# Optimization experiments

Hardware: AMD Instinct MI355X
Metric: run time of the kernel (lower is better)

The kernel has to match this reference:

```python
import jax, jax.numpy as jnp
import numpy as np

B, S, H, NH = 2, 1024, 1024, 16
SE, E = 512, 1024
NEXP, TOPK, FF = 8, 2, 2048
HD = H // NH
EPS = 1e-6
THETA = 10000.0
NEG = -1e9


def _rms(x, w):
    return x * jax.lax.rsqrt(jnp.mean(x * x, axis=-1, keepdims=True) + EPS) * w


def _rope(q, k, pos):
    # q,k: [B,S,NH,HD]; pos: [B,S] int
    inv = 1.0 / (THETA ** (jnp.arange(0, HD, 2, dtype=jnp.float32) / HD))
    f = pos[..., None].astype(jnp.float32) * inv            # [B,S,HD/2]
    emb = jnp.concatenate([f, f], axis=-1)                  # [B,S,HD]
    cos = jnp.cos(emb)[:, :, None, :]
    sin = jnp.sin(emb)[:, :, None, :]
    def rot(x):
        x1, x2 = jnp.split(x, 2, axis=-1)
        return jnp.concatenate([-x2, x1], axis=-1)
    return q * cos + rot(q) * sin, k * cos + rot(k) * sin


def _forward(hidden_states, encoder_hidden_states,
             in_ln_w, wq, wk, wv, wo,
             c_norm_w, cq_w, cq_b, ck_w, ck_b, cv_w, cv_b, co_w, co_b,
             post_ln_w, gate_w, w1, w2, w3,
             position_ids, encoder_attention_mask):
    x = hidden_states

    # ---- self-attention (RMSNorm pre-norm, RoPE, causal) ----
    res = x
    h = _rms(x, in_ln_w)
    q = (h @ wq.T).reshape(B, S, NH, HD)
    k = (h @ wk.T).reshape(B, S, NH, HD)
    v = (h @ wv.T).reshape(B, S, NH, HD)
    q, k = _rope(q, k, position_ids)
    scores = jnp.einsum('bqhd,bkhd->bhqk', q, k) / np.sqrt(HD)
    causal = jnp.tril(jnp.ones((S, S), dtype=bool))
    scores = jnp.where(causal, scores, NEG)
    attn = jax.nn.softmax(scores, axis=-1)
    o = jnp.einsum('bhqk,bkhd->bqhd', attn, v).reshape(B, S, H) @ wo.T
    x = res + o

    # ---- cross-attention block (RMSNorm, MHA with kdim=vdim=E, bias) ----
    res = x
    h = _rms(x, c_norm_w)
    cq = (h @ cq_w.T + cq_b).reshape(B, S, NH, HD)
    ck = (encoder_hidden_states @ ck_w.T + ck_b).reshape(B, SE, NH, HD)
    cv = (encoder_hidden_states @ cv_w.T + cv_b).reshape(B, SE, NH, HD)
    sc = jnp.einsum('bqhd,bkhd->bhqk', cq, ck) / np.sqrt(HD)
    pad = (encoder_attention_mask == 0)                     # key_padding_mask
    sc = jnp.where(pad[:, None, None, :], NEG, sc)
    ca = jax.nn.softmax(sc, axis=-1)
    o = jnp.einsum('bhqk,bkhd->bqhd', ca, cv).reshape(B, S, H) @ co_w.T + co_b
    x = res + o

    # ---- block-sparse MoE FFN (top-2 routing, SwiGLU experts) ----
    res = x
    h = _rms(x, post_ln_w).reshape(-1, H)                   # [T,H], T=B*S
    logits = h @ gate_w.T                                    # [T,NEXP]
    probs = jax.nn.softmax(logits, axis=-1)
    topv, topi = jax.lax.top_k(probs, TOPK)                  # [T,TOPK]
    topv = topv / jnp.sum(topv, axis=-1, keepdims=True)
    out = jnp.zeros_like(h)
    for e in range(NEXP):  # fixed small expert loop
        we = jnp.sum(jnp.where(topi == e, topv, 0.0), axis=-1)   # [T]
        ff = (jax.nn.silu(h @ w1[e].T) * (h @ w3[e].T)) @ w2[e].T
        out = out + we[:, None] * ff
    x = res + out.reshape(B, S, H)
    return x


def setup_inputs() -> dict:
    key = jax.random.key(0)
    ks = jax.random.split(key, 24)
    sc = 0.02
    d = {
        'hidden_states': jax.random.normal(ks[0], (B, S, H), jnp.float32),
        'position_ids': jnp.broadcast_to(jnp.arange(S, dtype=jnp.int64), (B, S)),
        'encoder_hidden_states': jax.random.normal(ks[1], (B, SE, E), jnp.float32),
        'encoder_attention_mask': jnp.ones((B, SE), jnp.int64),
        'in_ln_w': jnp.ones((H,), jnp.float32),
        'wq': jax.random.normal(ks[2], (H, H), jnp.float32) * sc,
        'wk': jax.random.normal(ks[3], (H, H), jnp.float32) * sc,
        'wv': jax.random.normal(ks[4], (H, H), jnp.float32) * sc,
        'wo': jax.random.normal(ks[5], (H, H), jnp.float32) * sc,
        'c_norm_w': jnp.ones((H,), jnp.float32),
        'cq_w': jax.random.normal(ks[6], (H, H), jnp.float32) * sc,
        'cq_b': jnp.zeros((H,), jnp.float32),
        'ck_w': jax.random.normal(ks[7], (H, E), jnp.float32) * sc,
        'ck_b': jnp.zeros((H,), jnp.float32),
        'cv_w': jax.random.normal(ks[8], (H, E), jnp.float32) * sc,
        'cv_b': jnp.zeros((H,), jnp.float32),
        'co_w': jax.random.normal(ks[9], (H, H), jnp.float32) * sc,
        'co_b': jnp.zeros((H,), jnp.float32),
        'post_ln_w': jnp.ones((H,), jnp.float32),
        'gate_w': jax.random.normal(ks[10], (NEXP, H), jnp.float32) * sc,
        'w1': jax.random.normal(ks[11], (NEXP, FF, H), jnp.float32) * sc,
        'w2': jax.random.normal(ks[12], (NEXP, H, FF), jnp.float32) * sc,
        'w3': jax.random.normal(ks[13], (NEXP, FF, H), jnp.float32) * sc,
    }
    return d


def reference(hidden_states, position_ids, encoder_hidden_states, encoder_attention_mask,
              in_ln_w, wq, wk, wv, wo,
              c_norm_w, cq_w, cq_b, ck_w, ck_b, cv_w, cv_b, co_w, co_b,
              post_ln_w, gate_w, w1, w2, w3):
    return _forward(hidden_states, encoder_hidden_states,
                    in_ln_w, wq, wk, wv, wo,
                    c_norm_w, cq_w, cq_b, ck_w, ck_b, cv_w, cv_b, co_w, co_b,
                    post_ln_w, gate_w, w1, w2, w3,
                    position_ids, encoder_attention_mask)
```

## Files before the change

### kernel.cpp

```cpp
#include <hip/hip_runtime.h>

#define B_    2
#define S_    1024
#define H_    1024
#define NH_   16
#define HD_   64
#define SE_   512
#define E_    1024
#define NEXP_ 8
#define FF_   2048
#define T_    (B_*S_)
#define TE_   (B_*SE_)
#define PERM_MAX 6400
#define MAXRT 24

typedef short v8s __attribute__((ext_vector_type(8)));
typedef short v4s __attribute__((ext_vector_type(4)));
typedef float v4f __attribute__((ext_vector_type(4)));
typedef _Float16 v8h __attribute__((ext_vector_type(8)));
typedef _Float16 v4h __attribute__((ext_vector_type(4)));

__device__ __forceinline__ unsigned short f2b(float f) {
  unsigned int u = __float_as_uint(f);
  u = (u + 0x7FFFu + ((u >> 16) & 1u)) >> 16;
  return (unsigned short)u;
}

__device__ __forceinline__ void g2l16(const void* g, void* l) {
  __builtin_amdgcn_global_load_lds(
      (const __attribute__((address_space(1))) unsigned int*)g,
      (__attribute__((address_space(3))) unsigned int*)l, 16, 0, 0);
}

__global__ void detect_kern(const int* __restrict__ pos, const int* __restrict__ msk,
                            int* __restrict__ flags, int* __restrict__ counts) {
  if (threadIdx.x < 16) counts[threadIdx.x] = 0;
  if (threadIdx.x == 0) {
    flags[0] = (pos[1] == 1) ? 0 : 1;
    flags[1] = (msk[1] == 1) ? 0 : 1;
  }
}

struct SplitArgs {
  const float* src[9];
  _Float16* dh[9];
  _Float16* dl[9];
};
__global__ __launch_bounds__(256)
void split_all(SplitArgs sa) {
  int b = blockIdx.x;
  int seg, i;
  if (b < 4096) { seg = b >> 9; i = (b & 511) * 256 + threadIdx.x; }
  else          { seg = 8;      i = (b - 4096) * 256 + threadIdx.x; }
  const float* x = sa.src[seg];
  v4f a = *(const v4f*)&x[i * 8];
  v4f c = *(const v4f*)&x[i * 8 + 4];
  v8h hv, lv;
  #pragma unroll
  for (int j = 0; j < 8; ++j) {
    float v = j < 4 ? a[j] : c[j - 4];
    _Float16 hh = (_Float16)v;
    hv[j] = hh; lv[j] = (_Float16)(v - (float)hh);
  }
  *(v8h*)&sa.dh[seg][i * 8] = hv;
  *(v8h*)&sa.dl[seg][i * 8] = lv;
}

__global__ __launch_bounds__(256)
void rmsnorm_hl_kern(const float* __restrict__ x, const float* __restrict__ w,
                     _Float16* __restrict__ yh, _Float16* __restrict__ yl) {
  int row = blockIdx.x, tid = threadIdx.x;
  const float* xr = x + (long)row * 1024;
  v4f v = *(const v4f*)&xr[tid * 4];
  float ss = v[0]*v[0] + v[1]*v[1] + v[2]*v[2] + v[3]*v[3];
  #pragma unroll
  for (int off = 32; off; off >>= 1) ss += __shfl_xor(ss, off);
  __shared__ float sw[4];
  if ((tid & 63) == 0) sw[tid >> 6] = ss;
  __syncthreads();
  float tot = sw[0] + sw[1] + sw[2] + sw[3];
  float rs = rsqrtf(tot * (1.0f / 1024.0f) + 1e-6f);
  const float* wr = w + tid * 4;
  v4h oh, ol;
  #pragma unroll
  for (int j = 0; j < 4; ++j) {
    float f = v[j] * rs * wr[j];
    _Float16 hh = (_Float16)f;
    oh[j] = hh; ol[j] = (_Float16)(f - (float)hh);
  }
  *(v4h*)&yh[(long)row * 1024 + tid * 4] = oh;
  *(v4h*)&yl[(long)row * 1024 + tid * 4] = ol;
}

__global__ __launch_bounds__(256)
void rmsnorm_kern(const float* __restrict__ x, const float* __restrict__ w,
                  unsigned short* __restrict__ y) {
  int row = blockIdx.x, tid = threadIdx.x;
  const float* xr = x + (long)row * 1024;
  v4f v = *(const v4f*)&xr[tid * 4];
  float ss = v[0]*v[0] + v[1]*v[1] + v[2]*v[2] + v[3]*v[3];
  #pragma unroll
  for (int off = 32; off; off >>= 1) ss += __shfl_xor(ss, off);
  __shared__ float sw[4];
  if ((tid & 63) == 0) sw[tid >> 6] = ss;
  __syncthreads();
  float tot = sw[0] + sw[1] + sw[2] + sw[3];
  float rs = rsqrtf(tot * (1.0f / 1024.0f) + 1e-6f);
  const float* wr = w + tid * 4;
  v4s o;
  #pragma unroll
  for (int j = 0; j < 4; ++j) o[j] = (short)f2b(v[j] * rs * wr[j]);
  *(v4s*)&y[(long)row * 1024 + tid * 4] = o;
}

__global__ __launch_bounds__(256)
void rope_split_kern(float* __restrict__ q, const float* __restrict__ k,
                     _Float16* __restrict__ kh, _Float16* __restrict__ kl,
                     const int* __restrict__ pos, const int* __restrict__ flags) {
  int g = blockIdx.x * 256 + threadIdx.x;
  int d = g & 31;
  int h = (g >> 5) & 15;
  int s = (g >> 9) & (S_ - 1);
  int b = g >> 19;
  long base = (((long)(b * S_ + s)) * NH_ + h) * HD_;
  int pidx = b * S_ + s;
  int pv = pos[flags[0] ? (pidx << 1) : pidx];
  float p = (float)pv;
  float inv = powf(10000.0f, -(float)d * (1.0f / 32.0f));
  float f = p * inv;
  float sn = sinf(f), cs = cosf(f);
  float q1 = q[base + d], q2 = q[base + d + 32];
  q[base + d]      = q1 * cs - q2 * sn;
  q[base + d + 32] = q2 * cs + q1 * sn;
  float k1 = k[base + d], k2 = k[base + d + 32];
  float kr1 = k1 * cs - k2 * sn;
  float kr2 = k2 * cs + k1 * sn;
  _Float16 hh = (_Float16)kr1;
  kh[base + d] = hh; kl[base + d] = (_Float16)(kr1 - (float)hh);
  hh = (_Float16)kr2;
  kh[base + d + 32] = hh; kl[base + d + 32] = (_Float16)(kr2 - (float)hh);
}

__global__ __launch_bounds__(256)
void vtrans_kern(const float* __restrict__ vf, _Float16* __restrict__ vth,
                 _Float16* __restrict__ vtl, int Sk) {
  int kb = blockIdx.x, bh = blockIdx.y;
  int b = bh >> 4, h = bh & 15;
  int t = threadIdx.x;
  __shared__ float tile[64][65];
  int key = t >> 2, dsub = (t & 3) * 16;
  const float* src = vf + (((long)(b * Sk + kb * 64 + key)) * NH_ + h) * HD_ + dsub;
  #pragma unroll
  for (int j = 0; j < 16; j += 4) *(v4f*)&tile[key][dsub + j] = *(const v4f*)&src[j];
  __syncthreads();
  int d = t >> 2, ksub = (t & 3) * 16;
  v8h hv0, lv0, hv1, lv1;
  #pragma unroll
  for (int j = 0; j < 16; ++j) {
    float v = tile[ksub + j][d];
    _Float16 hh = (_Float16)v;
    if (j < 8) { hv0[j] = hh; lv0[j] = (_Float16)(v - (float)hh); }
    else       { hv1[j - 8] = hh; lv1[j - 8] = (_Float16)(v - (float)hh); }
  }
  long ob = (((long)(b * NH_ + h)) * HD_ + d) * Sk + kb * 64 + ksub;
  *(v8h*)&vth[ob] = hv0; *(v8h*)&vth[ob + 8] = hv1;
  *(v8h*)&vtl[ob] = lv0; *(v8h*)&vtl[ob + 8] = lv1;
}

struct ZArg {
  const _Float16 *Ah, *Al, *Bh, *Bl;
  const float *bias, *resid;
  float *Cf;
  float *Cf2;
  _Float16 *Ch, *Cl;
  int M;
};

__global__ __launch_bounds__(256)
void gemm_hl(ZArg z0, ZArg z1, ZArg z2, int K) {
  ZArg za = blockIdx.z == 0 ? z0 : (blockIdx.z == 1 ? z1 : z2);
  int flat = blockIdx.x;
  int wg = (flat & 7) * 32 + (flat >> 3);
  int row0 = (wg >> 4) * 128;
  int col0 = (wg & 15) * 64;
  if (row0 >= za.M) return;
  int tid = threadIdx.x, lane = tid & 63, w = tid >> 6;
  int lr = lane & 15, lg = lane >> 4;
  int wr = w >> 1, wc = w & 1;
  int rsw = (lr >> 1) & 3;

  __shared__ _Float16 Ah_s[2][128 * 32], Al_s[2][128 * 32];
  __shared__ _Float16 Bh_s[2][64 * 32], Bl_s[2][64 * 32];

  int av0 = w * 64 + lane, av1 = (w + 4) * 64 + lane;
  int ar0 = av0 >> 2, as0 = (av0 & 3) ^ ((ar0 >> 1) & 3);
  int ar1 = av1 >> 2, as1 = (av1 & 3) ^ ((ar1 >> 1) & 3);
  int bv = w * 64 + lane;
  int br = bv >> 2, bs = (bv & 3) ^ ((br >> 1) & 3);
  const _Float16* ga0h = za.Ah + (long)(row0 + ar0) * K + as0 * 8;
  const _Float16* ga0l = za.Al + (long)(row0 + ar0) * K + as0 * 8;
  const _Float16* ga1h = za.Ah + (long)(row0 + ar1) * K + as1 * 8;
  const _Float16* ga1l = za.Al + (long)(row0 + ar1) * K + as1 * 8;
  const _Float16* gbh  = za.Bh + (long)(col0 + br) * K + bs * 8;
  const _Float16* gbl  = za.Bl + (long)(col0 + br) * K + bs * 8;

  auto stage = [&](int buf, int k0) {
    g2l16(ga0h + k0, (char*)Ah_s[buf] + w * 1024);
    g2l16(ga1h + k0, (char*)Ah_s[buf] + (w + 4) * 1024);
    g2l16(ga0l + k0, (char*)Al_s[buf] + w * 1024);
    g2l16(ga1l + k0, (char*)Al_s[buf] + (w + 4) * 1024);
    g2l16(gbh + k0, (char*)Bh_s[buf] + w * 1024);
    g2l16(gbl + k0, (char*)Bl_s[buf] + w * 1024);
  };

  v4f acc[4][2] = {};
  stage(0, 0);
  int cur = 0;

  for (int k0 = 0; k0 < K; k0 += 32) {
    __syncthreads();
    if (k0 + 32 < K) stage(cur ^ 1, k0 + 32);

    v8h ah[4], al[4], bh[2], bl[2];
    #pragma unroll
    for (int m = 0; m < 4; ++m) {
      int off = (wr * 64 + m * 16 + lr) * 64 + ((lg ^ rsw) << 4);
      ah[m] = *(const v8h*)((char*)Ah_s[cur] + off);
      al[m] = *(const v8h*)((char*)Al_s[cur] + off);
    }
    #pragma unroll
    for (int n = 0; n < 2; ++n) {
      int off = (wc * 32 + n * 16 + lr) * 64 + ((lg ^ rsw) << 4);
      bh[n] = *(const v8h*)((char*)Bh_s[cur] + off);
      bl[n] = *(const v8h*)((char*)Bl_s[cur] + off);
    }
    #pragma unroll
    for (int m = 0; m < 4; ++m)
      #pragma unroll
      for (int n = 0; n < 2; ++n) {
        acc[m][n] = __builtin_amdgcn_mfma_f32_16x16x32_f16(ah[m], bh[n], acc[m][n], 0, 0, 0);
        acc[m][n] = __builtin_amdgcn_mfma_f32_16x16x32_f16(ah[m], bl[n], acc[m][n], 0, 0, 0);
        acc[m][n] = __builtin_amdgcn_mfma_f32_16x16x32_f16(al[m], bh[n], acc[m][n], 0, 0, 0);
      }
    cur ^= 1;
  }

  #pragma unroll
  for (int m = 0; m < 4; ++m) {
    int rbase = row0 + wr * 64 + m * 16 + lg * 4;
    #pragma unroll
    for (int n = 0; n < 2; ++n) {
      int gcol = col0 + wc * 32 + n * 16 + lr;
      float bb = za.bias ? za.bias[gcol] : 0.0f;
      #pragma unroll
      for (int rr = 0; rr < 4; ++rr) {
        long idx = (long)(rbase + rr) * 1024 + gcol;
        float v = acc[m][n][rr] + bb;
        if (za.Cf) {
          float r = za.resid ? (za.resid[idx] + v) : v;
          za.Cf[idx] = r;
          if (za.Cf2) za.Cf2[idx] = r;
        } else {
          _Float16 hh = (_Float16)v;
          za.Ch[idx] = hh;
          za.Cl[idx] = (_Float16)(v - (float)hh);
        }
      }
    }
  }
}

template<bool CAUSAL>
__global__ __launch_bounds__(256)
void attn_hl(const float* __restrict__ Q,
             const _Float16* __restrict__ Khg, const _Float16* __restrict__ Klg,
             const _Float16* __restrict__ Vhg, const _Float16* __restrict__ Vlg,
             _Float16* __restrict__ Oh, _Float16* __restrict__ Ol,
             const int* __restrict__ mask, const int* __restrict__ flags,
             int Sq, int Sk, float qscale) {
  int flat = blockIdx.x;
  int wgA = (flat & 7) * 64 + (flat >> 3);
  int qt = wgA & 15, bh = wgA >> 4;
  int b = bh >> 4, h = bh & 15;
  int tid = threadIdx.x, lane = tid & 63, w = tid >> 6;
  int lr = lane & 15, lg = lane >> 4;
  int q0 = qt * 64;
  int mf = (!CAUSAL && mask) ? flags[1] : 0;
  int swz = lr & 7;

  __shared__ _Float16 Kh_s[64 * 64], Kl_s[64 * 64];
  __shared__ _Float16 Vh_s[64 * 64], Vl_s[64 * 64];
  __shared__ _Float16 Psh[4][16][72], Psl[4][16][72];

  v8h qh[2], ql[2];
  {
    long qbase = ((long)(b * Sq + q0 + w * 16 + lr) * NH_ + h) * HD_;
    #pragma unroll
    for (int kk = 0; kk < 2; ++kk) {
      v4f f0 = *(const v4f*)&Q[qbase + kk * 32 + lg * 8];
      v4f f1 = *(const v4f*)&Q[qbase + kk * 32 + lg * 8 + 4];
      #pragma unroll
      for (int j = 0; j < 8; ++j) {
        float f = (j < 4 ? f0[j] : f1[j - 4]) * qscale;
        _Float16 hh = (_Float16)f;
        qh[kk][j] = hh;
        ql[kk][j] = (_Float16)(f - (float)hh);
      }
    }
  }
  v4f of[4] = {};
  float m4[4], l4[4];
  #pragma unroll
  for (int i = 0; i < 4; ++i) { m4[i] = -3e38f; l4[i] = 0.0f; }

  int nkt = CAUSAL ? (qt + 1) : (Sk >> 6);
  for (int kt = 0; kt < nkt; ++kt) {
    __syncthreads();
    #pragma unroll
    for (int i = 0; i < 2; ++i) {
      int c = w + i * 4;
      int v = c * 64 + lane;
      int row = v >> 3, c8 = v & 7;
      int sc = (c8 ^ (row & 7)) << 3;
      long kb = ((long)(b * Sk + kt * 64 + row) * NH_ + h) * HD_ + sc;
      g2l16(Khg + kb, (char*)Kh_s + c * 1024);
      g2l16(Klg + kb, (char*)Kl_s + c * 1024);
      long vb = ((long)(b * NH_ + h) * HD_ + row) * Sk + kt * 64 + sc;
      g2l16(Vhg + vb, (char*)Vh_s + c * 1024);
      g2l16(Vlg + vb, (char*)Vl_s + c * 1024);
    }
    __syncthreads();

    v4f sf[4] = {};
    #pragma unroll
    for (int kk = 0; kk < 2; ++kk)
      #pragma unroll
      for (int n = 0; n < 4; ++n) {
        int off = (n * 16 + lr) * 128 + ((((kk << 2) | lg) ^ swz) << 4);
        v8h kbh = *(const v8h*)((char*)Kh_s + off);
        v8h kbl = *(const v8h*)((char*)Kl_s + off);
        sf[n] = __builtin_amdgcn_mfma_f32_16x16x32_f16(qh[kk], kbh, sf[n], 0, 0, 0);
        sf[n] = __builtin_amdgcn_mfma_f32_16x16x32_f16(qh[kk], kbl, sf[n], 0, 0, 0);
        sf[n] = __builtin_amdgcn_mfma_f32_16x16x32_f16(ql[kk], kbh, sf[n], 0, 0, 0);
      }

    if constexpr (CAUSAL) {
      if (kt == qt) {
        #pragma unroll
        for (int n = 0; n < 4; ++n) {
          int kcol = kt * 64 + n * 16 + lr;
          #pragma unroll
          for (int rr = 0; rr < 4; ++rr) {
            int qr = q0 + w * 16 + lg * 4 + rr;
            if (kcol > qr) sf[n][rr] = -1e9f;
          }
        }
      }
    } else {
      if (mask) {
        #pragma unroll
        for (int n = 0; n < 4; ++n) {
          int kcol = kt * 64 + n * 16 + lr;
          int mi = b * Sk + kcol;
          if (mask[mf ? (mi << 1) : mi] == 0) {
            #pragma unroll
            for (int rr = 0; rr < 4; ++rr) sf[n][rr] = -1e9f;
          }
        }
      }
    }

    float al[4];
    #pragma unroll
    for (int rr = 0; rr < 4; ++rr) {
      float mx = fmaxf(fmaxf(sf[0][rr], sf[1][rr]), fmaxf(sf[2][rr], sf[3][rr]));
      #pragma unroll
      for (int off = 8; off; off >>= 1) mx = fmaxf(mx, __shfl_xor(mx, off));
      float mn = fmaxf(m4[rr], mx);
      al[rr] = __expf(m4[rr] - mn);
      m4[rr] = mn;
      float rs = 0.0f;
      #pragma unroll
      for (int n = 0; n < 4; ++n) {
        float pv = __expf(sf[n][rr] - mn);
        sf[n][rr] = pv;
        rs += pv;
      }
      #pragma unroll
      for (int off = 8; off; off >>= 1) rs += __shfl_xor(rs, off);
      l4[rr] = l4[rr] * al[rr] + rs;
    }

    #pragma unroll
    for (int n = 0; n < 4; ++n)
      #pragma unroll
      for (int rr = 0; rr < 4; ++rr) {
        of[n][rr] *= al[rr];
        float pv = sf[n][rr];
        _Float16 ph = (_Float16)pv;
        Psh[w][lg * 4 + rr][n * 16 + lr] = ph;
        Psl[w][lg * 4 + rr][n * 16 + lr] = (_Float16)(pv - (float)ph);
      }
    __syncthreads();

    #pragma unroll
    for (int kc = 0; kc < 2; ++kc) {
      v8h pah = *(const v8h*)&Psh[w][lr][kc * 32 + lg * 8];
      v8h pal = *(const v8h*)&Psl[w][lr][kc * 32 + lg * 8];
      #pragma unroll
      for (int n = 0; n < 4; ++n) {
        int off = (n * 16 + lr) * 128 + ((((kc << 2) | lg) ^ swz) << 4);
        v8h vbh = *(const v8h*)((char*)Vh_s + off);
        v8h vbl = *(const v8h*)((char*)Vl_s + off);
        of[n] = __builtin_amdgcn_mfma_f32_16x16x32_f16(pah, vbh, of[n], 0, 0, 0);
        of[n] = __builtin_amdgcn_mfma_f32_16x16x32_f16(pah, vbl, of[n], 0, 0, 0);
        of[n] = __builtin_amdgcn_mfma_f32_16x16x32_f16(pal, vbh, of[n], 0, 0, 0);
      }
    }
  }

  #pragma unroll
  for (int rr = 0; rr < 4; ++rr) {
    int qr = q0 + w * 16 + lg * 4 + rr;
    float inv = 1.0f / l4[rr];
    long ob = (long)(b * Sq + qr) * 1024 + h * 64;
    #pragma unroll
    for (int n = 0; n < 4; ++n) {
      float v = of[n][rr] * inv;
      _Float16 hh = (_Float16)v;
      Oh[ob + n * 16 + lr] = hh;
      Ol[ob + n * 16 + lr] = (_Float16)(v - (float)hh);
    }
  }
}

__global__ __launch_bounds__(512)
void moe_gemm1(const unsigned short* __restrict__ A,
               const float* __restrict__ B1,
               const float* __restrict__ B2,
               unsigned short* __restrict__ Cb,
               const int* __restrict__ tm_e, const int* __restrict__ tm_slot,
               const int* __restrict__ ntl, const int* __restrict__ perm) {
  int flat = blockIdx.x;
  int wg = (flat & 7) * 96 + (flat >> 3);
  int tile = wg >> 5;
  if (tile >= ntl[0]) return;
  int col0 = (wg & 31) * 64;
  int e = tm_e[tile];
  int row0 = tm_slot[tile];
  const float* Bp1 = B1 + (long)e * (FF_ * H_);
  const float* Bp2 = B2 + (long)e * (FF_ * H_);
  int tid = threadIdx.x, lane = tid & 63, w = tid >> 6;
  int lr = lane & 15, lg = lane >> 4;
  int wr = w >> 1, wc = w & 1;
  int rsw = (lr >> 1) & 3;

  __shared__ unsigned short As[2][256 * 32];
  __shared__ unsigned short Bs1[2][64 * 32];
  __shared__ unsigned short Bs2[2][64 * 32];

  const unsigned short* ga[2];
  #pragma unroll
  for (int i = 0; i < 2; ++i) {
    int c = i * 512 + tid;
    int r = c >> 2, sub = (c & 3) ^ ((r >> 1) & 3);
    int tok = perm[row0 + r];
    ga[i] = A + (long)(tok < 0 ? 0 : tok) * H_ + sub * 8;
  }
  int bc = tid & 255;
  int rb = bc >> 2, sb = (bc & 3) ^ ((rb >> 1) & 3);
  const float* gB = (tid < 256 ? Bp1 : Bp2) + (long)(col0 + rb) * H_ + sb * 8;
  int lBoff = bc * 8;

  auto stage = [&](int buf, int k0) {
    v4f b0 = *(const v4f*)&gB[k0];
    v4f b1 = *(const v4f*)&gB[k0 + 4];
    #pragma unroll
    for (int i = 0; i < 2; ++i)
      g2l16(ga[i] + k0, As[buf] + (size_t)(i * 512 + w * 64) * 8);
    v8s hv;
    #pragma unroll
    for (int j = 0; j < 8; ++j) hv[j] = (short)f2b(j < 4 ? b0[j] : b1[j - 4]);
    *(v8s*)&((tid < 256 ? Bs1 : Bs2)[buf][lBoff]) = hv;
  };

  v4f acc[4][2] = {};
  v4f acc2[4][2] = {};
  stage(0, 0);
  int cur = 0;

  for (int k0 = 0; k0 < H_; k0 += 32) {
    __syncthreads();
    if (k0 + 32 < H_) stage(cur ^ 1, k0 + 32);

    v8s a[4], b1v[2], b2v[2];
    #pragma unroll
    for (int m = 0; m < 4; ++m)
      a[m] = *(const v8s*)&As[cur][(wr * 64 + m * 16 + lr) * 32 + (lg ^ rsw) * 8];
    #pragma unroll
    for (int n = 0; n < 2; ++n) {
      b1v[n] = *(const v8s*)&Bs1[cur][(wc * 32 + n * 16 + lr) * 32 + (lg ^ rsw) * 8];
      b2v[n] = *(const v8s*)&Bs2[cur][(wc * 32 + n * 16 + lr) * 32 + (lg ^ rsw) * 8];
    }
    #pragma unroll
    for (int m = 0; m < 4; ++m)
      #pragma unroll
      for (int n = 0; n < 2; ++n) {
        acc[m][n]  = __builtin_amdgcn_mfma_f32_16x16x32_bf16(a[m], b1v[n], acc[m][n], 0, 0, 0);
        acc2[m][n] = __builtin_amdgcn_mfma_f32_16x16x32_bf16(a[m], b2v[n], acc2[m][n], 0, 0, 0);
      }
    cur ^= 1;
  }

  #pragma unroll
  for (int m = 0; m < 4; ++m) {
    int grow = row0 + wr * 64 + m * 16 + lg * 4;
    #pragma unroll
    for (int n = 0; n < 2; ++n) {
      int gcol = col0 + wc * 32 + n * 16 + lr;
      #pragma unroll
      for (int rr = 0; rr < 4; ++rr) {
        float v = acc[m][n][rr];
        float g = v / (1.0f + __expf(-v));
        Cb[(long)(grow + rr) * FF_ + gcol] = f2b(g * acc2[m][n][rr]);
      }
    }
  }
}

__global__ __launch_bounds__(256)
void moe_gemm2(const unsigned short* __restrict__ A,
               const float* __restrict__ B,
               float* __restrict__ Cf,
               const int* __restrict__ tm_e, const int* __restrict__ tm_slot,
               const int* __restrict__ ntl,
               const int* __restrict__ perm, const float* __restrict__ pwgt) {
  int flat = blockIdx.x;
  int wg = (flat & 7) * 96 + (flat >> 3);
  int t2 = wg >> 4;
  int tile = t2 >> 1;
  if (tile >= ntl[0]) return;
  int row0 = tm_slot[tile] + (t2 & 1) * 128;
  int col0 = (wg & 15) * 64;
  int e = tm_e[tile];
  const float* Bp = B + (long)e * (H_ * FF_);
  int tid = threadIdx.x, lane = tid & 63, w = tid >> 6;
  int lr = lane & 15, lg = lane >> 4;
  int rsw = (lr >> 1) & 3;

  __shared__ unsigned short As[2][128 * 32];
  __shared__ unsigned short Bs[2][64 * 32];

  const unsigned short* ga[2];
  #pragma unroll
  for (int i = 0; i < 2; ++i) {
    int c = i * 256 + tid;
    int r = c >> 2, sub = (c & 3) ^ ((r >> 1) & 3);
    ga[i] = A + (long)(row0 + r) * FF_ + sub * 8;
  }
  int rb = tid >> 2, sb = (tid & 3) ^ ((rb >> 1) & 3);
  const float* gb = Bp + (long)(col0 + rb) * FF_ + sb * 8;
  int lBoff = tid * 8;

  auto stage = [&](int buf, int k0) {
    v4f b0 = *(const v4f*)&gb[k0];
    v4f b1 = *(const v4f*)&gb[k0 + 4];
    #pragma unroll
    for (int i = 0; i < 2; ++i)
      g2l16(ga[i] + k0, As[buf] + (size_t)(i * 256 + w * 64) * 8);
    v8s hv;
    #pragma unroll
    for (int j = 0; j < 8; ++j) hv[j] = (short)f2b(j < 4 ? b0[j] : b1[j - 4]);
    *(v8s*)&Bs[buf][lBoff] = hv;
  };

  v4f acc[2][4] = {};
  stage(0, 0);
  int cur = 0;

  for (int k0 = 0; k0 < FF_; k0 += 32) {
    __syncthreads();
    if (k0 + 32 < FF_) stage(cur ^ 1, k0 + 32);

    v8s a[2], b[4];
    #pragma unroll
    for (int m = 0; m < 2; ++m)
      a[m] = *(const v8s*)&As[cur][(w * 32 + m * 16 + lr) * 32 + (lg ^ rsw) * 8];
    #pragma unroll
    for (int n = 0; n < 4; ++n)
      b[n] = *(const v8s*)&Bs[cur][(n * 16 + lr) * 32 + (lg ^ rsw) * 8];
    #pragma unroll
    for (int m = 0; m < 2; ++m)
      #pragma unroll
      for (int n = 0; n < 4; ++n)
        acc[m][n] = __builtin_amdgcn_mfma_f32_16x16x32_bf16(a[m], b[n], acc[m][n], 0, 0, 0);
    cur ^= 1;
  }

  #pragma unroll
  for (int m = 0; m < 2; ++m) {
    int grow = row0 + w * 32 + m * 16 + lg * 4;
    #pragma unroll
    for (int rr = 0; rr < 4; ++rr) {
      int tok = perm[grow + rr];
      if (tok < 0) continue;
      float pw = pwgt[grow + rr];
      #pragma unroll
      for (int n = 0; n < 4; ++n) {
        int gcol = col0 + n * 16 + lr;
        atomicAdd(&Cf[(long)tok * H_ + gcol], acc[m][n][rr] * pw);
      }
    }
  }
}

__global__ __launch_bounds__(64)
void router_kern(const float* __restrict__ x, const float* __restrict__ w,
                 const float* __restrict__ gw,
                 int* __restrict__ topi, float* __restrict__ topw,
                 int* __restrict__ counts) {
  int t = blockIdx.x, lane = threadIdx.x;
  const float* xr = x + (long)t * 1024;
  float vals[16];
  float ss = 0.0f;
  #pragma unroll
  for (int i = 0; i < 16; ++i) { float v = xr[lane + i * 64]; vals[i] = v; ss += v * v; }
  #pragma unroll
  for (int off = 32; off; off >>= 1) ss += __shfl_xor(ss, off);
  float rs = rsqrtf(ss * (1.0f / 1024.0f) + 1e-6f);
  #pragma unroll
  for (int i = 0; i < 16; ++i) vals[i] *= rs * w[lane + i * 64];
  float lgts[8];
  #pragma unroll
  for (int e = 0; e < 8; ++e) {
    const float* g = gw + e * 1024;
    float s = 0.0f;
    #pragma unroll
    for (int i = 0; i < 16; ++i) s += vals[i] * g[lane + i * 64];
    #pragma unroll
    for (int off = 32; off; off >>= 1) s += __shfl_xor(s, off);
    lgts[e] = s;
  }
  int i1 = 0; float l1 = lgts[0];
  #pragma unroll
  for (int e = 1; e < 8; ++e) if (lgts[e] > l1) { l1 = lgts[e]; i1 = e; }
  int i2 = -1; float l2 = -3e38f;
  #pragma unroll
  for (int e = 0; e < 8; ++e) if (e != i1 && lgts[e] > l2) { l2 = lgts[e]; i2 = e; }
  float w1 = 1.0f / (1.0f + __expf(l2 - l1));
  if (lane == 0) {
    topi[t * 2] = i1; topi[t * 2 + 1] = i2;
    topw[t * 2] = w1; topw[t * 2 + 1] = 1.0f - w1;
    atomicAdd(&counts[i1], 1);
    atomicAdd(&counts[i2], 1);
  }
}

__global__ __launch_bounds__(256)
void route_pack_kern(const int* __restrict__ counts,
                     const int* __restrict__ topi, const float* __restrict__ topw,
                     int* __restrict__ poff,
                     int* __restrict__ tm_e, int* __restrict__ tm_slot,
                     int* __restrict__ ntl,
                     int* __restrict__ perm, float* __restrict__ pwgt) {
  __shared__ int s_poff[8];
  __shared__ int s_cur[8];
  __shared__ int stot;
  if (threadIdx.x < 8) s_cur[threadIdx.x] = 0;
  if (threadIdx.x == 0) {
    int off = 0, nt = 0;
    for (int e = 0; e < 8; ++e) {
      s_poff[e] = off; poff[e] = off;
      int c = counts[e];
      int ntE = (c + 255) >> 8;
      for (int i = 0; i < ntE; ++i) { tm_e[nt] = e; tm_slot[nt] = off + i * 256; ++nt; }
      off += ntE * 256;
    }
    ntl[0] = nt; ntl[1] = off;
    stot = off;
  }
  __syncthreads();
  for (int s = threadIdx.x; s < stot; s += 256) perm[s] = -1;
  __syncthreads();
  for (int t = threadIdx.x; t < T_; t += 256) {
    #pragma unroll
    for (int kk = 0; kk < 2; ++kk) {
      int e = topi[t * 2 + kk];
      int pos = atomicAdd(&s_cur[e], 1);
      int slot = s_poff[e] + pos;
      perm[slot] = t;
      pwgt[slot] = topw[t * 2 + kk];
    }
  }
}

extern "C" void kernel_launch(void* const* d_in, const int* in_sizes, int n_in,
                              void* d_out, int out_size, void* d_ws, size_t ws_size,
                              hipStream_t stream) {
  (void)in_sizes; (void)n_in; (void)out_size; (void)ws_size;
  const float* x_in  = (const float*)d_in[0];
  const int*  posids = (const int*)d_in[1];
  const float* enc   = (const float*)d_in[2];
  const int*  emask  = (const int*)d_in[3];
  const float* inln  = (const float*)d_in[4];
  const float* wq    = (const float*)d_in[5];
  const float* wk    = (const float*)d_in[6];
  const float* wv    = (const float*)d_in[7];
  const float* wo    = (const float*)d_in[8];
  const float* cnorm = (const float*)d_in[9];
  const float* cqw   = (const float*)d_in[10];
  const float* cqb   = (const float*)d_in[11];
  const float* ckw   = (const float*)d_in[12];
  const float* ckb   = (const float*)d_in[13];
  const float* cvw   = (const float*)d_in[14];
  const float* cvb   = (const float*)d_in[15];
  const float* cow   = (const float*)d_in[16];
  const float* cob   = (const float*)d_in[17];
  const float* pln   = (const float*)d_in[18];
  const float* gatew = (const float*)d_in[19];
  const float* w1    = (const float*)d_in[20];
  const float* w2    = (const float*)d_in[21];
  const float* w3    = (const float*)d_in[22];
  float* out = (float*)d_out;

  char* p = (char*)d_ws;
  auto alloc = [&](size_t bytes) -> char* {
    char* r = p;
    p += (bytes + 255) & ~(size_t)255;
    return r;
  };
  const size_t MB = 1024 * 1024;
  char* A1 = alloc(4 * MB);
  char* A2 = alloc(4 * MB);
  char* Bq = alloc(8 * MB);
  char* Bk = alloc(8 * MB);
  char* Bv = alloc(8 * MB);
  char* C1 = alloc(4 * MB);
  char* C2 = alloc(4 * MB);
  char* D1 = alloc(4 * MB);
  char* D2 = alloc(4 * MB);
  float* x1 = (float*)alloc(8 * MB);
  float* x2 = (float*)alloc(8 * MB);
  unsigned short* h3b = (unsigned short*)alloc(4 * MB);
  _Float16* ench = (_Float16*)alloc(2 * MB);
  _Float16* encl = (_Float16*)alloc(2 * MB);
  int*   meta    = (int*)alloc(4 * (8 + 8 + 8 + 2 + 2 + MAXRT + MAXRT));
  int*   counts  = meta;
  int*   poff    = meta + 16;
  int*   ntl     = meta + 24;
  int*   flags   = meta + 26;
  int*   tm_e    = meta + 28;
  int*   tm_slot = meta + 28 + MAXRT;
  int*   topi    = (int*)alloc((size_t)T_ * 2 * 4);
  float* topw    = (float*)alloc((size_t)T_ * 2 * 4);
  int*   perm    = (int*)alloc((size_t)PERM_MAX * 4);
  float* pwgt    = (float*)alloc((size_t)PERM_MAX * 4);
  _Float16* wsp  = (_Float16*)alloc(32 * MB);

  _Float16 *hh = (_Float16*)A1, *hl = (_Float16*)A2;
  _Float16 *oh = (_Float16*)A1, *ol = (_Float16*)A2;
  _Float16 *ckh = (_Float16*)A1, *ckl = (_Float16*)A2;
  float* qf = (float*)Bq;  float* cqf = (float*)Bq;
  float* kf = (float*)Bk;
  _Float16 *cvth = (_Float16*)Bk, *cvtl = (_Float16*)(Bk + 4 * MB);
  float* vf = (float*)Bv;  float* cvf = (float*)Bv;
  _Float16 *kh = (_Float16*)C1, *kl = (_Float16*)C2;
  _Float16 *h2h = (_Float16*)C1, *h2l = (_Float16*)C2;
  _Float16 *vth = (_Float16*)D1, *vtl = (_Float16*)D2;
  _Float16 *coh = (_Float16*)D1, *col = (_Float16*)D2;
  unsigned short* ffh = (unsigned short*)Bq;
  auto wsph = [&](int i) { return wsp + (size_t)i * 2097152; };
  auto wspl = [&](int i) { return wsp + (size_t)i * 2097152 + 1048576; };

  dim3 blk(256);

  detect_kern<<<1, 64, 0, stream>>>(posids, emask, flags, counts);

  {
    SplitArgs sa;
    const float* wlist[8] = {wq, wk, wv, wo, cqw, ckw, cvw, cow};
    for (int i = 0; i < 8; ++i) { sa.src[i] = wlist[i]; sa.dh[i] = wsph(i); sa.dl[i] = wspl(i); }
    sa.src[8] = enc; sa.dh[8] = ench; sa.dl[8] = encl;
    split_all<<<4608, blk, 0, stream>>>(sa);
  }

  rmsnorm_hl_kern<<<T_, blk, 0, stream>>>(x_in, inln, hh, hl);
  {
    ZArg zq = {hh, hl, wsph(0), wspl(0), nullptr, nullptr, qf, nullptr, nullptr, nullptr, 2048};
    ZArg zk = {hh, hl, wsph(1), wspl(1), nullptr, nullptr, kf, nullptr, nullptr, nullptr, 2048};
    ZArg zv = {hh, hl, wsph(2), wspl(2), nullptr, nullptr, vf, nullptr, nullptr, nullptr, 2048};
    gemm_hl<<<dim3(256, 1, 3), blk, 0, stream>>>(zq, zk, zv, 1024);
  }
  rope_split_kern<<<(B_ * S_ * NH_ * 32) / 256, blk, 0, stream>>>(qf, kf, kh, kl, posids, flags);
  vtrans_kern<<<dim3(16, 32), blk, 0, stream>>>(vf, vth, vtl, 1024);
  attn_hl<true><<<512, blk, 0, stream>>>(
      qf, kh, kl, vth, vtl, oh, ol, nullptr, flags, 1024, 1024, 0.125f);
  {
    ZArg zo = {oh, ol, wsph(3), wspl(3), nullptr, x_in, x1, nullptr, nullptr, nullptr, 2048};
    gemm_hl<<<dim3(256, 1, 1), blk, 0, stream>>>(zo, zo, zo, 1024);
  }

  rmsnorm_hl_kern<<<T_, blk, 0, stream>>>(x1, cnorm, h2h, h2l);
  {
    ZArg zcq = {h2h, h2l, wsph(4), wspl(4), cqb, nullptr, cqf, nullptr, nullptr, nullptr, 2048};
    ZArg zck = {ench, encl, wsph(5), wspl(5), ckb, nullptr, nullptr, nullptr, ckh, ckl, 1024};
    ZArg zcv = {ench, encl, wsph(6), wspl(6), cvb, nullptr, cvf, nullptr, nullptr, nullptr, 1024};
    gemm_hl<<<dim3(256, 1, 3), blk, 0, stream>>>(zcq, zck, zcv, 1024);
  }
  vtrans_kern<<<dim3(8, 32), blk, 0, stream>>>(cvf, cvth, cvtl, 512);
  attn_hl<false><<<512, blk, 0, stream>>>(
      cqf, ckh, ckl, cvth, cvtl, coh, col, emask, flags, 1024, 512, 0.125f);
  {
    ZArg zco = {coh, col, wsph(7), wspl(7), cob, x1, x2, out, nullptr, nullptr, 2048};
    gemm_hl<<<dim3(256, 1, 1), blk, 0, stream>>>(zco, zco, zco, 1024);
  }

  rmsnorm_kern<<<T_, blk, 0, stream>>>(x2, pln, h3b);
  router_kern<<<T_, dim3(64), 0, stream>>>(x2, pln, gatew, topi, topw, counts);
  route_pack_kern<<<1, blk, 0, stream>>>(counts, topi, topw, poff, tm_e, tm_slot,
                                         ntl, perm, pwgt);
  moe_gemm1<<<768, dim3(512), 0, stream>>>(
      h3b, w1, w3, ffh, tm_e, tm_slot, ntl, perm);
  moe_gemm2<<<768, blk, 0, stream>>>(
      ffh, w2, out, tm_e, tm_slot, ntl, perm, pwgt);
}
```

Baseline: 550.8 us.

## Prefetch fp32 expert weights into registers one stage ahead in MoE GEMMs

Both MoE expert GEMM kernels now issue the global fp32 weight loads for the tile two steps ahead into registers, then convert to bf16 and write shared memory after the MFMA step. Before, each load was converted right away. The main loop is unrolled by two with alternating register buffers, so the global load latency is hidden behind MFMA work instead of stalling the conversion. This costs more registers and keeps the loop-carried prefetch state explicit.

```diff
diff --git a/kernel.cpp b/kernel.cpp
--- a/kernel.cpp
+++ b/kernel.cpp
@@ -470,37 +470,43 @@
   int bc = tid & 255;
   int rb = bc >> 2, sb = (bc & 3) ^ ((rb >> 1) & 3);
   const float* gB = (tid < 256 ? Bp1 : Bp2) + (long)(col0 + rb) * H_ + sb * 8;
-  int lBoff = bc * 8;
-
-  auto stage = [&](int buf, int k0) {
-    v4f b0 = *(const v4f*)&gB[k0];
-    v4f b1 = *(const v4f*)&gB[k0 + 4];
+  unsigned short* lB0 = &((tid < 256 ? Bs1 : Bs2)[0][bc * 8]);
+  unsigned short* lB1 = &((tid < 256 ? Bs1 : Bs2)[1][bc * 8]);
+
+  auto g2lA = [&](int buf, int k0) {
     #pragma unroll
     for (int i = 0; i < 2; ++i)
       g2l16(ga[i] + k0, As[buf] + (size_t)(i * 512 + w * 64) * 8);
+  };
+  auto cvtw = [&](unsigned short* dst, v4f b0, v4f b1) {
     v8s hv;
     #pragma unroll
     for (int j = 0; j < 8; ++j) hv[j] = (short)f2b(j < 4 ? b0[j] : b1[j - 4]);
-    *(v8s*)&((tid < 256 ? Bs1 : Bs2)[buf][lBoff]) = hv;
+    *(v8s*)dst = hv;
   };
 
   v4f acc[4][2] = {};
   v4f acc2[4][2] = {};
-  stage(0, 0);
+
+  {
+    v4f t0 = *(const v4f*)&gB[0];
+    v4f t1 = *(const v4f*)&gB[4];
+    cvtw(lB0, t0, t1);
+  }
+  g2lA(0, 0);
+  v4f pA0 = *(const v4f*)&gB[32], pA1 = *(const v4f*)&gB[36];
+  v4f pB0, pB1;
   int cur = 0;
 
-  for (int k0 = 0; k0 < H_; k0 += 32) {
-    __syncthreads();
-    if (k0 + 32 < H_) stage(cur ^ 1, k0 + 32);
-
+  auto mfma_step = [&](int c) {
     v8s a[4], b1v[2], b2v[2];
     #pragma unroll
     for (int m = 0; m < 4; ++m)
-      a[m] = *(const v8s*)&As[cur][(wr * 64 + m * 16 + lr) * 32 + (lg ^ rsw) * 8];
+      a[m] = *(const v8s*)&As[c][(wr * 64 + m * 16 + lr) * 32 + (lg ^ rsw) * 8];
     #pragma unroll
     for (int n = 0; n < 2; ++n) {
-      b1v[n] = *(const v8s*)&Bs1[cur][(wc * 32 + n * 16 + lr) * 32 + (lg ^ rsw) * 8];
-      b2v[n] = *(const v8s*)&Bs2[cur][(wc * 32 + n * 16 + lr) * 32 + (lg ^ rsw) * 8];
+      b1v[n] = *(const v8s*)&Bs1[c][(wc * 32 + n * 16 + lr) * 32 + (lg ^ rsw) * 8];
+      b2v[n] = *(const v8s*)&Bs2[c][(wc * 32 + n * 16 + lr) * 32 + (lg ^ rsw) * 8];
     }
     #pragma unroll
     for (int m = 0; m < 4; ++m)
@@ -509,6 +515,20 @@
         acc[m][n]  = __builtin_amdgcn_mfma_f32_16x16x32_bf16(a[m], b1v[n], acc[m][n], 0, 0, 0);
         acc2[m][n] = __builtin_amdgcn_mfma_f32_16x16x32_bf16(a[m], b2v[n], acc2[m][n], 0, 0, 0);
       }
+  };
+
+  for (int k0 = 0; k0 < H_; k0 += 64) {
+    __syncthreads();
+    if (k0 + 32 < H_) g2lA(cur ^ 1, k0 + 32);
+    if (k0 + 64 < H_) { pB0 = *(const v4f*)&gB[k0 + 64]; pB1 = *(const v4f*)&gB[k0 + 68]; }
+    mfma_step(cur);
+    if (k0 + 32 < H_) cvtw(cur ? lB0 : lB1, pA0, pA1);
+    cur ^= 1;
+    __syncthreads();
+    if (k0 + 64 < H_) g2lA(cur ^ 1, k0 + 64);
+    if (k0 + 96 < H_) { pA0 = *(const v4f*)&gB[k0 + 96]; pA1 = *(const v4f*)&gB[k0 + 100]; }
+    mfma_step(cur);
+    if (k0 + 64 < H_) cvtw(cur ? lB0 : lB1, pB0, pB1);
     cur ^= 1;
   }
 
@@ -560,40 +580,60 @@
   }
   int rb = tid >> 2, sb = (tid & 3) ^ ((rb >> 1) & 3);
   const float* gb = Bp + (long)(col0 + rb) * FF_ + sb * 8;
-  int lBoff = tid * 8;
-
-  auto stage = [&](int buf, int k0) {
-    v4f b0 = *(const v4f*)&gb[k0];
-    v4f b1 = *(const v4f*)&gb[k0 + 4];
+  unsigned short* lB0 = &Bs[0][tid * 8];
+  unsigned short* lB1 = &Bs[1][tid * 8];
+
+  auto g2lA = [&](int buf, int k0) {
     #pragma unroll
     for (int i = 0; i < 2; ++i)
       g2l16(ga[i] + k0, As[buf] + (size_t)(i * 256 + w * 64) * 8);
+  };
+  auto cvtw = [&](unsigned short* dst, v4f b0, v4f b1) {
     v8s hv;
     #pragma unroll
     for (int j = 0; j < 8; ++j) hv[j] = (short)f2b(j < 4 ? b0[j] : b1[j - 4]);
-    *(v8s*)&Bs[buf][lBoff] = hv;
+    *(v8s*)dst = hv;
   };
 
   v4f acc[2][4] = {};
-  stage(0, 0);
+
+  {
+    v4f t0 = *(const v4f*)&gb[0];
+    v4f t1 = *(const v4f*)&gb[4];
+    cvtw(lB0, t0, t1);
+  }
+  g2lA(0, 0);
+  v4f pA0 = *(const v4f*)&gb[32], pA1 = *(const v4f*)&gb[36];
+  v4f pB0, pB1;
   int cur = 0;
 
-  for (int k0 = 0; k0 < FF_; k0 += 32) {
-    __syncthreads();
-    if (k0 + 32 < FF_) stage(cur ^ 1, k0 + 32);
-
+  auto mfma_step = [&](int c) {
     v8s a[2], b[4];
     #pragma unroll
     for (int m = 0; m < 2; ++m)
-      a[m] = *(const v8s*)&As[cur][(w * 32 + m * 16 + lr) * 32 + (lg ^ rsw) * 8];
+      a[m] = *(const v8s*)&As[c][(w * 32 + m * 16 + lr) * 32 + (lg ^ rsw) * 8];
     #pragma unroll
     for (int n = 0; n < 4; ++n)
-      b[n] = *(const v8s*)&Bs[cur][(n * 16 + lr) * 32 + (lg ^ rsw) * 8];
+      b[n] = *(const v8s*)&Bs[c][(n * 16 + lr) * 32 + (lg ^ rsw) * 8];
     #pragma unroll
     for (int m = 0; m < 2; ++m)
       #pragma unroll
       for (int n = 0; n < 4; ++n)
         acc[m][n] = __builtin_amdgcn_mfma_f32_16x16x32_bf16(a[m], b[n], acc[m][n], 0, 0, 0);
+  };
+
+  for (int k0 = 0; k0 < FF_; k0 += 64) {
+    __syncthreads();
+    if (k0 + 32 < FF_) g2lA(cur ^ 1, k0 + 32);
+    if (k0 + 64 < FF_) { pB0 = *(const v4f*)&gb[k0 + 64]; pB1 = *(const v4f*)&gb[k0 + 68]; }
+    mfma_step(cur);
+    if (k0 + 32 < FF_) cvtw(cur ? lB0 : lB1, pA0, pA1);
+    cur ^= 1;
+    __syncthreads();
+    if (k0 + 64 < FF_) g2lA(cur ^ 1, k0 + 64);
+    if (k0 + 96 < FF_) { pA0 = *(const v4f*)&gb[k0 + 96]; pA1 = *(const v4f*)&gb[k0 + 100]; }
+    mfma_step(cur);
+    if (k0 + 64 < FF_) cvtw(cur ? lB0 : lB1, pB0, pB1);
     cur ^= 1;
   }
 
```

Result: no change. 550.8 us (+0.0%).
